# Kernel optimization log

Hardware: AMD Instinct MI355X
Metric: run time of the kernel (lower is better)

## Reference

```python
import jax, jax.numpy as jnp
import numpy as np

K = 9            # connections per output pixel
GA = 2           # global additional samples
RA = 2           # relative additional samples
VS = 4 + GA + RA # 2^rank neighbours + sampled
REGION = 12      # int(0.25 * 48) per spatial dim
MMULT = 0.1
MIN_SIGMA = 0.05
SIGMA_SCALE = 0.05
SIGMA_BOOST = 2.0


def setup_inputs() -> dict:
    key = jax.random.key(0)
    ks = jax.random.split(key, 8)
    b, cin, h, w = 8, 128, 48, 48
    cout = 256
    hidden = cin * 4

    def lin_init(k, fan_out, fan_in):
        bound = 1.0 / np.sqrt(fan_in)
        kw, kb = jax.random.split(k)
        W = jax.random.uniform(kw, (fan_out, fan_in), minval=-bound, maxval=bound, dtype=jnp.float32)
        bb = jax.random.uniform(kb, (fan_out,), minval=-bound, maxval=bound, dtype=jnp.float32)
        return W, bb

    x = jax.random.normal(ks[0], (b, cin, h, w), dtype=jnp.float32)
    W1, b1 = lin_init(ks[1], hidden, 2)          # toparams layer 1 (adaptive=False -> 2 coord inputs)
    W2, b2 = lin_init(ks[2], 3 * K, hidden)      # toparams layer 2 -> k means (2d) + k sigmas
    Wu, bu = lin_init(ks[3], cout, K * cin)      # unify linear
    gints = jax.random.randint(ks[4], (b, h, w, K, GA, 2), 0, h, dtype=jnp.int32)      # global samples (h==w)
    roff = jax.random.randint(ks[5], (b, h, w, K, RA, 2), 0, REGION, dtype=jnp.int32)  # relative offsets
    return {"x": x, "W1": W1, "b1": b1, "W2": W2, "b2": b2, "Wu": Wu, "bu": bu,
            "gints": gints, "roff": roff}


def reference(x, W1, b1, W2, b2, Wu, bu, gints, roff):
    b, c, h, w = x.shape
    s = jnp.array([h, w], dtype=x.dtype)                       # spatial range per dim
    s_int = jnp.array([h, w], dtype=jnp.int32)

    # normalized coordinate grid in [0,1], (h, w, 2) with [.,.,0]=row, [.,.,1]=col
    rows = jnp.arange(h, dtype=x.dtype) / (h - 1)
    cols = jnp.arange(w, dtype=x.dtype) / (w - 1)
    coords = jnp.stack(jnp.meshgrid(rows, cols, indexing='ij'), axis=-1)

    # hypernetwork: per-pixel coords -> K 2d mean offsets + K sigmas
    inp = jnp.broadcast_to(coords, (b, h, w, 2))
    hid = jax.nn.relu(inp @ W1.T + b1)
    params = hid @ W2.T + b2                                   # (b,h,w,3K)
    means_raw = params[..., :2 * K].reshape(b, h, w, K, 2)
    sig_raw = params[..., 2 * K:]                              # (b,h,w,K)

    # mids: inverse of the sigmoid scaling applied to the pixel's own coordinate
    pix = coords * (s - 1)                                     # pixel coordinates
    sc = pix / (s - 1) * 0.9999 + 0.00005
    mids = jnp.log(sc / (1.0 - sc))                            # (h,w,2)

    # transform_means: sigmoid -> [0, s-1]
    means = jax.nn.sigmoid(mids[None, :, :, None, :] + MMULT * means_raw) * (s - 1)  # (b,h,w,K,2)
    # transform_sigmas: softplus(. + boost) + min, per-dim scale, then sigma_scale
    sigmas = (jax.nn.softplus(sig_raw + SIGMA_BOOST) + MIN_SIGMA)[..., None] * s * SIGMA_SCALE  # (b,h,w,K,2)

    # ---- integer index generation (non-differentiable) ----
    fl = jnp.floor(jax.lax.stop_gradient(means)).astype(jnp.int32)   # (b,h,w,K,2)
    combos = jnp.array([[0, 0], [0, 1], [1, 0], [1, 1]], dtype=jnp.int32)
    neigh = fl[..., None, :] + combos                                 # (b,h,w,K,4,2)
    rel = fl[..., None, :] + roff - REGION // 2                       # (b,h,w,K,RA,2)
    ints = jnp.concatenate([neigh, gints, rel], axis=-2) % s_int      # (b,h,w,K,VS,2)

    # duplicate masking: zero any tuple that occurred earlier along VS
    eq = jnp.all(ints[..., :, None, :] == ints[..., None, :, :], axis=-1)  # (...,VS,VS)
    lower = jnp.tril(jnp.ones((VS, VS), dtype=bool), k=-1)
    dups = jnp.any(eq & lower, axis=-1)                               # (b,h,w,K,VS)

    # unnormalized gaussian densities of integer points under (means, sigmas)
    diff = (ints.astype(x.dtype) - means[..., None, :]) / sigmas[..., None, :]
    props = jnp.exp(-0.5 * jnp.sum(diff * diff, axis=-1))             # (b,h,w,K,VS)
    props = jnp.where(dups, jnp.zeros((), x.dtype), props)
    weights = props / jnp.sum(props, axis=-1, keepdims=True)          # mvalues are all-ones

    # irregular gather of input channel vectors at sampled pixels
    lin = ints[..., 0] * w + ints[..., 1]                             # (b,h,w,K,VS)
    flat = x.transpose(0, 2, 3, 1).reshape(b, h * w, c)
    feats = flat[jnp.arange(b)[:, None], lin.reshape(b, -1)]          # (b, h*w*K*VS, c)
    feats = feats.reshape(b, h, w, K, VS, c)

    feats = jnp.einsum('bhwkvc,bhwkv->bhwkc', feats, weights)         # weighted reduce over VS
    feats = feats.reshape(b, h, w, K * c)
    out = feats @ Wu.T + bu                                           # unify linear
    return out.transpose(0, 3, 1, 2)                                  # (b, cout, h, w)
```

## Files before the change

### kernel.cpp

```cpp
#include <hip/hip_runtime.h>
#include <hip/hip_bf16.h>
#include <hip/hip_fp16.h>

#define BB 8
#define CIN 128
#define HH 48
#define WW 48
#define HW 2304
#define KK 9
#define COUT 256
#define KC 1152
#define MM 18432
#define MT 32
#define SFP 136

#define LIGHT_BARRIER() asm volatile("s_waitcnt lgkmcnt(0)\n\ts_barrier" ::: "memory")

typedef short bf16x8_t __attribute__((ext_vector_type(8)));
typedef float f32x16_t __attribute__((ext_vector_type(16)));
typedef float f32x4_t  __attribute__((ext_vector_type(4)));

static __device__ __forceinline__ float b2f(short u) {
    union { unsigned int i; float f; } c;
    c.i = ((unsigned int)(unsigned short)u) << 16;
    return c.f;
}

__global__ __launch_bounds__(256) void prep_kernel(
    const float* __restrict__ x, __hip_bfloat16* __restrict__ xT,
    const float* __restrict__ Wu, bf16x8_t* __restrict__ Bp,
    const float* __restrict__ W1, const float* __restrict__ b1,
    const float* __restrict__ W2, const float* __restrict__ b2,
    float* __restrict__ means, float* __restrict__ sigmas, int* __restrict__ fls)
{
    int bid = blockIdx.x;
    int t = threadIdx.x;

    if (bid < 576) {
        __shared__ float tile[64][65];
        int ij0 = (bid % 36) * 64;
        int c0  = ((bid / 36) % 2) * 64;
        int b   = bid / 72;
        int ijl = t & 63, cl = t >> 6;
        #pragma unroll
        for (int i = 0; i < 16; i++) {
            int cc = i*4 + cl;
            tile[cc][ijl] = x[(size_t)(b*CIN + c0 + cc) * HW + ij0 + ijl];
        }
        __syncthreads();
        int cl2 = t & 63, ijl2 = t >> 6;
        #pragma unroll
        for (int i = 0; i < 16; i++) {
            int ij = i*4 + ijl2;
            xT[(size_t)(b*HW + ij0 + ij) * CIN + c0 + cl2] = __float2bfloat16(tile[cl2][ij]);
        }
    } else if (bid < 720) {
        int idx = (bid - 576) * 256 + t;
        int lane = idx & 63;
        int rest = idx >> 6;
        int s = rest % 72, g = rest / 72;
        int r = lane & 31, qq = lane >> 5;
        const float* src = Wu + (size_t)(g*32 + r) * KC + s*16 + qq*8;
        union { bf16x8_t v; __hip_bfloat16 h[8]; } o;
        #pragma unroll
        for (int j = 0; j < 8; j++) o.h[j] = __float2bfloat16(src[j]);
        Bp[idx] = o.v;
    } else {
        int wave = t >> 6, lane = t & 63;
        int p = (bid - 720) * 4 + wave;
        int iy = p / WW, ix = p % WW;
        float ryf = (float)iy / 47.0f;
        float rxf = (float)ix / 47.0f;
        double ry = (double)ryf, rx = (double)rxf;

        double h[8];
        #pragma unroll
        for (int jj = 0; jj < 8; jj++) {
            int j = lane*8 + jj;
            double v = ry * (double)W1[j*2+0] + rx * (double)W1[j*2+1] + (double)b1[j];
            h[jj] = v > 0.0 ? v : 0.0;
        }
        double par[27];
        #pragma unroll
        for (int o = 0; o < 27; o++) {
            const float4* w4 = (const float4*)(W2 + (size_t)o*512 + lane*8);
            float4 wa = w4[0], wb = w4[1];
            double s = (double)wa.x*h[0] + (double)wa.y*h[1]
                     + (double)wa.z*h[2] + (double)wa.w*h[3]
                     + (double)wb.x*h[4] + (double)wb.y*h[5]
                     + (double)wb.z*h[6] + (double)wb.w*h[7];
            par[o] = s;
        }
        #pragma unroll
        for (int o = 0; o < 27; o++) {
            #pragma unroll
            for (int d = 1; d < 64; d <<= 1)
                par[o] += __shfl_xor(par[o], d, 64);
            par[o] += (double)b2[o];
        }
        if (lane < KK) {
            int k = lane;
            double scy = ry * 0.9999 + 5e-05;
            double scx = rx * 0.9999 + 5e-05;
            double midy = log(scy / (1.0 - scy));
            double midx = log(scx / (1.0 - scx));
            double zy = midy + 0.1 * par[2*k+0];
            double zx = midx + 0.1 * par[2*k+1];
            double my = 47.0 / (1.0 + exp(-zy));
            double mx = 47.0 / (1.0 + exp(-zx));
            double sr = par[18 + k] + 2.0;
            double sp = (sr > 0.0 ? sr : 0.0) + log1p(exp(-fabs(sr)));
            double sg = (sp + 0.05) * 48.0 * 0.05;
            means[(p*KK + k)*2 + 0] = (float)my;
            means[(p*KK + k)*2 + 1] = (float)mx;
            sigmas[p*KK + k] = (float)sg;
            fls[(p*KK + k)*2 + 0] = (int)floor(my);
            fls[(p*KK + k)*2 + 1] = (int)floor(mx);
        }
    }
}

__global__ __launch_bounds__(512, 4) void fused_kernel(
    const float* __restrict__ means, const float* __restrict__ sigmas,
    const int* __restrict__ fls, const int* __restrict__ gints,
    const int* __restrict__ roff, const short* __restrict__ xT,
    const bf16x8_t* __restrict__ Bp, const float* __restrict__ bu,
    float* __restrict__ out)
{
    __shared__ unsigned int s_tap[KK*MT*8];
    __shared__ __align__(16) short s_feat[2][MT*SFP];

    int t = threadIdx.x;
    int b   = blockIdx.x & 7;
    int grp = blockIdx.x >> 3;
    int ij0 = grp * MT;
    int m0  = b * HW + ij0;

    if (t < KK*MT) {
        int p = t;
        int k = p >> 5, row = p & 31;
        int ij = ij0 + row;
        int bij = m0 + row;
        int fy = fls[(ij*KK + k)*2 + 0];
        int fx = fls[(ij*KK + k)*2 + 1];
        float my = means[(ij*KK + k)*2 + 0];
        float mx = means[(ij*KK + k)*2 + 1];
        float sg = sigmas[ij*KK + k];
        int lins[8]; float ws[8];
        #pragma unroll
        for (int v = 0; v < 8; v++) {
            int iy, ix;
            if (v < 4) {
                iy = fy + (v >> 1); ix = fx + (v & 1);
            } else if (v < 6) {
                int base = ((bij*KK + k)*2 + (v - 4)) * 2;
                iy = gints[base]; ix = gints[base + 1];
            } else {
                int base = ((bij*KK + k)*2 + (v - 6)) * 2;
                iy = fy + roff[base] - 6; ix = fx + roff[base + 1] - 6;
            }
            iy = ((iy % HH) + HH) % HH;
            ix = ((ix % WW) + WW) % WW;
            lins[v] = iy * WW + ix;
            float dy = ((float)iy - my) / sg;
            float dx = ((float)ix - mx) / sg;
            ws[v] = expf(-0.5f * (dy*dy + dx*dx));
        }
        #pragma unroll
        for (int v = 1; v < 8; v++) {
            bool dup = false;
            #pragma unroll
            for (int u = 0; u < 8; u++) if (u < v) dup = dup || (lins[u] == lins[v]);
            if (dup) ws[v] = 0.0f;
        }
        float sum = 0.0f;
        #pragma unroll
        for (int v = 0; v < 8; v++) sum += ws[v];
        float inv = 1.0f / sum;
        #pragma unroll
        for (int v = 0; v < 8; v++) {
            unsigned short hb = __half_as_ushort(__float2half(ws[v] * inv));
            s_tap[p*8+v] = ((unsigned int)lins[v] << 16) | (unsigned int)hb;
        }
    }
    LIGHT_BARRIER();

    const short* xb = xT + (size_t)b * (HW * CIN);
    int lane = t & 63, wave = t >> 6;
    int r = lane & 31, q = lane >> 5;
    int grow = t >> 4, gc0 = (t & 15) << 3;

    f32x16_t acc = {};

    bf16x8_t tap[8];
    float    wgt[8];
    {
        const unsigned int* tp = &s_tap[(0*MT + grow)*8];
        #pragma unroll
        for (int v = 0; v < 8; v++) {
            unsigned int e = tp[v];
            wgt[v] = __half2float(__ushort_as_half((unsigned short)(e & 0xffffu)));
            tap[v] = *(const bf16x8_t*)(xb + (size_t)(e >> 16) * CIN + gc0);
        }
    }

    for (int k = 0; k < KK; k++) {
        float a0[8];
        #pragma unroll
        for (int j = 0; j < 8; j++) a0[j] = 0.0f;
        #pragma unroll
        for (int v = 0; v < 8; v++) {
            float w = wgt[v]; bf16x8_t d8 = tap[v];
            #pragma unroll
            for (int j = 0; j < 8; j++) a0[j] += w * b2f(d8[j]);
        }
        bf16x8_t Bf[8];
        {
            int base = (wave*72 + k*8)*64 + lane;
            #pragma unroll
            for (int si = 0; si < 8; si++) Bf[si] = Bp[base + si*64];
        }
        if (k < KK - 1) {
            const unsigned int* tp = &s_tap[((k+1)*MT + grow)*8];
            #pragma unroll
            for (int v = 0; v < 8; v++) {
                unsigned int e = tp[v];
                wgt[v] = __half2float(__ushort_as_half((unsigned short)(e & 0xffffu)));
                tap[v] = *(const bf16x8_t*)(xb + (size_t)(e >> 16) * CIN + gc0);
            }
        }
        {
            union { bf16x8_t v8; __hip_bfloat16 hh[8]; } o;
            #pragma unroll
            for (int j = 0; j < 8; j++) o.hh[j] = __float2bfloat16(a0[j]);
            *(bf16x8_t*)(&s_feat[k & 1][grow*SFP + gc0]) = o.v8;
        }
        LIGHT_BARRIER();
        {
            const short* fb = s_feat[k & 1];
            #pragma unroll
            for (int si = 0; si < 8; si++) {
                bf16x8_t a = *(const bf16x8_t*)(fb + r*SFP + si*16 + q*8);
                acc = __builtin_amdgcn_mfma_f32_32x32x16_bf16(a, Bf[si], acc, 0, 0, 0);
            }
        }
    }

    int n = wave*32 + r;
    float bv = bu[n];
    float* oc = out + ((size_t)b * COUT + n) * HW + ij0;
    #pragma unroll
    for (int g4 = 0; g4 < 4; g4++) {
        f32x4_t vv;
        vv[0] = acc[g4*4+0] + bv;
        vv[1] = acc[g4*4+1] + bv;
        vv[2] = acc[g4*4+2] + bv;
        vv[3] = acc[g4*4+3] + bv;
        *(f32x4_t*)(oc + g4*8 + q*4) = vv;
    }
}

extern "C" void kernel_launch(void* const* d_in, const int* in_sizes, int n_in,
                              void* d_out, int out_size, void* d_ws, size_t ws_size,
                              hipStream_t stream)
{
    const float* x   = (const float*)d_in[0];
    const float* W1  = (const float*)d_in[1];
    const float* b1  = (const float*)d_in[2];
    const float* W2  = (const float*)d_in[3];
    const float* b2  = (const float*)d_in[4];
    const float* Wu  = (const float*)d_in[5];
    const float* bu  = (const float*)d_in[6];
    const int* gints = (const int*)d_in[7];
    const int* roff  = (const int*)d_in[8];
    float* out = (float*)d_out;

    char* ws = (char*)d_ws;
    float* ws_means  = (float*)(ws + 0);
    float* ws_sigma  = (float*)(ws + 165888);
    int*   ws_fl     = (int*  )(ws + 248832);
    short* ws_xT     = (short*)(ws + 414720);
    bf16x8_t* ws_bp  = (bf16x8_t*)(ws + 5133312);

    prep_kernel<<<1296, 256, 0, stream>>>(x, (__hip_bfloat16*)ws_xT, Wu, ws_bp,
                                          W1, b1, W2, b2,
                                          ws_means, ws_sigma, ws_fl);
    fused_kernel<<<MM/MT, 512, 0, stream>>>(ws_means, ws_sigma, ws_fl, gints, roff,
                                            ws_xT, ws_bp, bu, out);
}
```

Measured before the change: 153.5 us.

## Halve row tile to 16 and switch to 16x16x32 MFMA with 256-thread blocks

Reduces the per-block M tile from 32 to 16 rows, doubling the grid to 1152 blocks of 256 threads. The GEMM stage moves from 32x32x16 MFMAs to 16x16x32 MFMAs, with each wave covering four 16-column output tiles, and Wu is re-packed into a matching fragment layout. The aim is more blocks for better occupancy and load balance, and shorter per-block latency. In exchange, B-fragment loads are now inside the MFMA loop and amortised over half as many rows, so weight traffic per output row doubles.

Measured after the change: 151.0 us. About the same (-1.6%).

```diff
diff --git a/kernel.cpp b/kernel.cpp
--- a/kernel.cpp
+++ b/kernel.cpp
@@ -11,13 +11,12 @@
 #define COUT 256
 #define KC 1152
 #define MM 18432
-#define MT 32
+#define MT 16
 #define SFP 136
 
 #define LIGHT_BARRIER() asm volatile("s_waitcnt lgkmcnt(0)\n\ts_barrier" ::: "memory")
 
 typedef short bf16x8_t __attribute__((ext_vector_type(8)));
-typedef float f32x16_t __attribute__((ext_vector_type(16)));
 typedef float f32x4_t  __attribute__((ext_vector_type(4)));
 
 static __device__ __forceinline__ float b2f(short u) {
@@ -58,9 +57,9 @@
         int idx = (bid - 576) * 256 + t;
         int lane = idx & 63;
         int rest = idx >> 6;
-        int s = rest % 72, g = rest / 72;
-        int r = lane & 31, qq = lane >> 5;
-        const float* src = Wu + (size_t)(g*32 + r) * KC + s*16 + qq*8;
+        int ksub = rest % 36, tile16 = rest / 36;
+        const float* src = Wu + (size_t)(tile16*16 + (lane & 15)) * KC
+                              + ksub*32 + (lane >> 4)*8;
         union { bf16x8_t v; __hip_bfloat16 h[8]; } o;
         #pragma unroll
         for (int j = 0; j < 8; j++) o.h[j] = __float2bfloat16(src[j]);
@@ -120,7 +119,7 @@
     }
 }
 
-__global__ __launch_bounds__(512, 4) void fused_kernel(
+__global__ __launch_bounds__(256, 4) void fused_kernel(
     const float* __restrict__ means, const float* __restrict__ sigmas,
     const int* __restrict__ fls, const int* __restrict__ gints,
     const int* __restrict__ roff, const short* __restrict__ xT,
@@ -138,7 +137,7 @@
 
     if (t < KK*MT) {
         int p = t;
-        int k = p >> 5, row = p & 31;
+        int k = p >> 4, row = p & 15;
         int ij = ij0 + row;
         int bij = m0 + row;
         int fy = fls[(ij*KK + k)*2 + 0];
@@ -187,10 +186,10 @@
 
     const short* xb = xT + (size_t)b * (HW * CIN);
     int lane = t & 63, wave = t >> 6;
-    int r = lane & 31, q = lane >> 5;
     int grow = t >> 4, gc0 = (t & 15) << 3;
-
-    f32x16_t acc = {};
+    int arow = lane & 15, aq = lane >> 4;
+
+    f32x4_t acc[4] = {};
 
     bf16x8_t tap[8];
     float    wgt[8];
@@ -213,12 +212,6 @@
             float w = wgt[v]; bf16x8_t d8 = tap[v];
             #pragma unroll
             for (int j = 0; j < 8; j++) a0[j] += w * b2f(d8[j]);
-        }
-        bf16x8_t Bf[8];
-        {
-            int base = (wave*72 + k*8)*64 + lane;
-            #pragma unroll
-            for (int si = 0; si < 8; si++) Bf[si] = Bp[base + si*64];
         }
         if (k < KK - 1) {
             const unsigned int* tp = &s_tap[((k+1)*MT + grow)*8];
@@ -238,25 +231,32 @@
         LIGHT_BARRIER();
         {
             const short* fb = s_feat[k & 1];
-            #pragma unroll
-            for (int si = 0; si < 8; si++) {
-                bf16x8_t a = *(const bf16x8_t*)(fb + r*SFP + si*16 + q*8);
-                acc = __builtin_amdgcn_mfma_f32_32x32x16_bf16(a, Bf[si], acc, 0, 0, 0);
+            bf16x8_t av[4];
+            #pragma unroll
+            for (int s4 = 0; s4 < 4; s4++)
+                av[s4] = *(const bf16x8_t*)(fb + arow*SFP + s4*32 + aq*8);
+            #pragma unroll
+            for (int tl = 0; tl < 4; tl++) {
+                int fbase = ((wave*4 + tl)*36 + k*4)*64 + lane;
+                #pragma unroll
+                for (int s4 = 0; s4 < 4; s4++) {
+                    bf16x8_t Bf = Bp[fbase + s4*64];
+                    acc[tl] = __builtin_amdgcn_mfma_f32_16x16x32_bf16(av[s4], Bf, acc[tl], 0, 0, 0);
+                }
             }
         }
     }
 
-    int n = wave*32 + r;
-    float bv = bu[n];
-    float* oc = out + ((size_t)b * COUT + n) * HW + ij0;
     #pragma unroll
-    for (int g4 = 0; g4 < 4; g4++) {
+    for (int tl = 0; tl < 4; tl++) {
+        int n = (wave*4 + tl)*16 + arow;
+        float bv = bu[n];
         f32x4_t vv;
-        vv[0] = acc[g4*4+0] + bv;
-        vv[1] = acc[g4*4+1] + bv;
-        vv[2] = acc[g4*4+2] + bv;
-        vv[3] = acc[g4*4+3] + bv;
-        *(f32x4_t*)(oc + g4*8 + q*4) = vv;
+        vv[0] = acc[tl][0] + bv;
+        vv[1] = acc[tl][1] + bv;
+        vv[2] = acc[tl][2] + bv;
+        vv[3] = acc[tl][3] + bv;
+        *(f32x4_t*)(out + ((size_t)b * COUT + n) * HW + ij0 + aq*4) = vv;
     }
 }
 
@@ -285,6 +285,6 @@
     prep_kernel<<<1296, 256, 0, stream>>>(x, (__hip_bfloat16*)ws_xT, Wu, ws_bp,
                                           W1, b1, W2, b2,
                                           ws_means, ws_sigma, ws_fl);
-    fused_kernel<<<MM/MT, 512, 0, stream>>>(ws_means, ws_sigma, ws_fl, gints, roff,
+    fused_kernel<<<MM/MT, 256, 0, stream>>>(ws_means, ws_sigma, ws_fl, gints, roff,
                                             ws_xT, ws_bp, bu, out);
 }
```
